# Performance work log

Hardware: AMD Instinct MI355X
Metric: run time of the kernel (lower is better)

The kernel has to match this reference:

```python
import jax, jax.numpy as jnp
import numpy as np

L = 18                      # chain length -> Hilbert dim 2^L
J1 = 1.0                    # fixed exchange coupling (not trainable)
M_KRYLOV = 64               # Lanczos subspace size (>= n_eigs)
DIM = 2 ** L

# spin-1/2 operators (S = sigma/2)
SX = 0.5 * jnp.array([[0., 1.], [1., 0.]], jnp.float32)
SZ = 0.5 * jnp.array([[1., 0.], [0., -1.]], jnp.float32)
# two-site Heisenberg bond S_i.S_j in basis |00>,|01>,|10>,|11> (real: SxSx+SySy = flip terms)
BOND = jnp.array([[0.25, 0., 0., 0.],
                  [0., -0.25, 0.5, 0.],
                  [0., 0.5, -0.25, 0.],
                  [0., 0., 0., 0.25]], jnp.float32)


def setup_inputs() -> dict:
    key = jax.random.key(0)
    phi = jnp.asarray(2.0 * np.pi * np.arange(L) / L, jnp.float32)
    phi = phi + 0.01 * jax.random.normal(key, (L,), jnp.float32)
    return {
        "B_0": jnp.float32(0.2),
        "B_ext": jnp.float32(0.05),
        "phi_i": phi,
        "n_eigs": 4,
    }


def _matvec(v, field_ops):
    """Matrix-free H @ v for the open Heisenberg chain with site fields.
    v: (DIM,), field_ops: (L, 2, 2)."""
    out = jnp.zeros_like(v)
    bond = jnp.float32(J1) * BOND
    for i in range(L - 1):  # fixed structural loop over bonds
        blk = v.reshape(2 ** i, 4, 2 ** (L - i - 2))
        out = out + jnp.einsum('ab,xbz->xaz', bond, blk).reshape(-1)
    for i in range(L):      # fixed structural loop over sites (Zeeman term)
        blk = v.reshape(2 ** i, 2, 2 ** (L - i - 1))
        out = out + jnp.einsum('ab,xbz->xaz', field_ops[i], blk).reshape(-1)
    return out


def _lanczos(field_ops, v0, m):
    """m-step Lanczos; returns Krylov basis V (m, DIM) and tridiag coeffs."""
    def step(carry, _):
        v_prev, v, beta_prev = carry
        w = _matvec(v, field_ops)
        alpha = jnp.vdot(v, w)
        w = w - alpha * v - beta_prev * v_prev
        beta = jnp.sqrt(jnp.vdot(w, w))
        v_next = w / jnp.maximum(beta, jnp.float32(1e-12))
        return (v, v_next, beta), (v, alpha, beta)

    init = (jnp.zeros_like(v0), v0, jnp.float32(0.0))
    _, (V, alphas, betas) = jax.lax.scan(step, init, None, length=m)
    return V, alphas, betas


def reference(B_0, B_ext, phi_i, n_eigs):
    # skyrmion-texture field: in-plane/out-of-plane components from phi_i
    Bx = B_0 * jnp.sin(phi_i)
    Bz = B_0 * jnp.cos(phi_i) + B_ext
    field_ops = Bx[:, None, None] * SX + Bz[:, None, None] * SZ  # (L,2,2)

    v0 = jax.random.normal(jax.random.key(42), (DIM,), jnp.float32)  # v_init='randn'
    v0 = v0 / jnp.sqrt(jnp.vdot(v0, v0))

    V, a, b = _lanczos(field_ops, v0, M_KRYLOV)
    T = jnp.diag(a) + jnp.diag(b[:-1], 1) + jnp.diag(b[:-1], -1)  # (m,m) tridiag
    w, U = jnp.linalg.eigh(T)
    eigvals = w[:n_eigs]                                   # lowest n_eigs Ritz values
    eigvecs = jnp.einsum('md,mk->dk', V, U[:, :n_eigs])    # Ritz vectors (DIM, n_eigs)
    return eigvals, eigvecs
```

## Files before the change

kernel.cpp:

```cpp
#include <hip/hip_runtime.h>
#include <stdint.h>

#define L 18
#define DIM (1 << L)
#define MKRY 64
#define NBLK 256
#define TPB 1024

__device__ __forceinline__ uint32_t rotl32(uint32_t v, int r){ return (v<<r)|(v>>(32-r)); }

__device__ __forceinline__ void threefry2x32(uint32_t k0, uint32_t k1, uint32_t x0, uint32_t x1,
                                             uint32_t& o0, uint32_t& o1) {
  uint32_t k2 = k0 ^ k1 ^ 0x1BD11BDAu;
  x0 += k0; x1 += k1;
  x0+=x1; x1=rotl32(x1,13); x1^=x0;
  x0+=x1; x1=rotl32(x1,15); x1^=x0;
  x0+=x1; x1=rotl32(x1,26); x1^=x0;
  x0+=x1; x1=rotl32(x1,6);  x1^=x0;
  x0+=k1; x1+=k2+1u;
  x0+=x1; x1=rotl32(x1,17); x1^=x0;
  x0+=x1; x1=rotl32(x1,29); x1^=x0;
  x0+=x1; x1=rotl32(x1,16); x1^=x0;
  x0+=x1; x1=rotl32(x1,24); x1^=x0;
  x0+=k2; x1+=k0+2u;
  x0+=x1; x1=rotl32(x1,13); x1^=x0;
  x0+=x1; x1=rotl32(x1,15); x1^=x0;
  x0+=x1; x1=rotl32(x1,26); x1^=x0;
  x0+=x1; x1=rotl32(x1,6);  x1^=x0;
  x0+=k0; x1+=k1+3u;
  x0+=x1; x1=rotl32(x1,17); x1^=x0;
  x0+=x1; x1=rotl32(x1,29); x1^=x0;
  x0+=x1; x1=rotl32(x1,16); x1^=x0;
  x0+=x1; x1=rotl32(x1,24); x1^=x0;
  x0+=k1; x1+=k2+4u;
  x0+=x1; x1=rotl32(x1,13); x1^=x0;
  x0+=x1; x1=rotl32(x1,15); x1^=x0;
  x0+=x1; x1=rotl32(x1,26); x1^=x0;
  x0+=x1; x1=rotl32(x1,6);  x1^=x0;
  x0+=k2; x1+=k0+5u;
  o0=x0; o1=x1;
}

__device__ float jax_erfinv(float x){
  #pragma clang fp contract(off)
  float w = -log1pf(-x*x);
  float p;
  if (w < 5.0f) {
    w = w - 2.5f;
    p = 2.81022636e-08f;
    p = 3.43273939e-07f + p*w;
    p = -3.5233877e-06f + p*w;
    p = -4.39150654e-06f + p*w;
    p = 0.00021858087f + p*w;
    p = -0.00125372503f + p*w;
    p = -0.00417768164f + p*w;
    p = 0.246640727f + p*w;
    p = 1.50140941f + p*w;
  } else {
    w = sqrtf(w) - 3.0f;
    p = -0.000200214257f;
    p = 0.000100950558f + p*w;
    p = 0.00134934322f + p*w;
    p = -0.00367342844f + p*w;
    p = 0.00573950773f + p*w;
    p = -0.0076224613f + p*w;
    p = 0.00943887047f + p*w;
    p = 1.00167406f + p*w;
    p = 2.83297682f + p*w;
  }
  return p*x;
}

__device__ __forceinline__ float rng_val(unsigned i){
  #pragma clang fp contract(off)
  uint32_t o0,o1; threefry2x32(0u,42u,0u,i,o0,o1);
  uint32_t bits = o0 ^ o1;
  float f = __uint_as_float((bits >> 9) | 0x3f800000u) - 1.0f;
  const float lo = -0.99999994f;
  float u = f*2.0f;
  u = u + lo;
  u = fmaxf(lo, u);
  return 1.41421354f * jax_erfinv(u);
}

__device__ __forceinline__ double2 blockReduce2(double a, double b){
  __shared__ double sa[16], sb[16], res[2];
  int lane = threadIdx.x & 63, wid = threadIdx.x >> 6;
  #pragma unroll
  for (int off=32; off; off>>=1){ a += __shfl_down(a,off,64); b += __shfl_down(b,off,64); }
  if (lane==0){ sa[wid]=a; sb[wid]=b; }
  __syncthreads();
  if (wid==0){
    double xa = (lane<16)? sa[lane] : 0.0;
    double xb = (lane<16)? sb[lane] : 0.0;
    #pragma unroll
    for (int off=8; off; off>>=1){ xa += __shfl_down(xa,off,64); xb += __shfl_down(xb,off,64); }
    if (lane==0){ res[0]=xa; res[1]=xb; }
  }
  __syncthreads();
  double2 r; r.x=res[0]; r.y=res[1];
  return r;
}

__device__ __forceinline__ void gbar2(unsigned* bar, unsigned epoch){
  __syncthreads();
  if (threadIdx.x==0){
    const int st = (blockIdx.x & 7)*32;
    __hip_atomic_fetch_add(&bar[st], 1u, __ATOMIC_ACQ_REL, __HIP_MEMORY_SCOPE_AGENT);
    if (blockIdx.x==0){
      unsigned guard=0;
      for (;;){
        unsigned sum=0;
        #pragma unroll
        for (int k=0;k<8;++k)
          sum += __hip_atomic_load(&bar[k*32], __ATOMIC_ACQUIRE, __HIP_MEMORY_SCOPE_AGENT);
        if (sum >= (unsigned)NBLK) break;
        __builtin_amdgcn_s_sleep(1);
        if (++guard > (1u<<22)) break;
      }
      #pragma unroll
      for (int k=0;k<8;++k)
        __hip_atomic_store(&bar[k*32], 0u, __ATOMIC_RELAXED, __HIP_MEMORY_SCOPE_AGENT);
      __hip_atomic_fetch_add(&bar[256], 1u, __ATOMIC_RELEASE, __HIP_MEMORY_SCOPE_AGENT);
    } else {
      unsigned guard=0;
      while (__hip_atomic_load(&bar[256], __ATOMIC_RELAXED, __HIP_MEMORY_SCOPE_AGENT) < epoch){
        __builtin_amdgcn_s_sleep(1);
        if (++guard > (1u<<22)) break;
      }
      (void)__hip_atomic_load(&bar[256], __ATOMIC_ACQUIRE, __HIP_MEMORY_SCOPE_AGENT);
    }
  }
  __syncthreads();
}

__device__ __forceinline__ void gbar_arrive_spin0(unsigned* bar){
  const int st = (blockIdx.x & 7)*32;
  __hip_atomic_fetch_add(&bar[st], 1u, __ATOMIC_ACQ_REL, __HIP_MEMORY_SCOPE_AGENT);
  if (blockIdx.x==0){
    unsigned guard=0;
    for (;;){
      unsigned sum=0;
      #pragma unroll
      for (int k=0;k<8;++k)
        sum += __hip_atomic_load(&bar[k*32], __ATOMIC_ACQUIRE, __HIP_MEMORY_SCOPE_AGENT);
      if (sum >= (unsigned)NBLK) break;
      __builtin_amdgcn_s_sleep(1);
      if (++guard > (1u<<22)) break;
    }
    #pragma unroll
    for (int k=0;k<8;++k)
      __hip_atomic_store(&bar[k*32], 0u, __ATOMIC_RELAXED, __HIP_MEMORY_SCOPE_AGENT);
  }
}

#define CM_INIT {3u<<16,3u<<15,3u<<14,3u<<13,3u<<12,3u<<11,3u<<10,3u<<9, \
                 1u<<17,1u<<16,1u<<15,1u<<14,1u<<13,1u<<12,1u<<11,1u<<10}

__device__ __forceinline__ float matvec1(int s, int tid, float vs,
                                         const float* __restrict__ lds_v,
                                         const float2 (*__restrict__ lds_h)[TPB],
                                         const float* __restrict__ hxz){
  #pragma clang fp contract(off)
  float acc = 0.0f;
  #pragma unroll
  for (int i=0;i<L-1;++i){
    const int q = L-2-i;
    const unsigned msk = 3u<<q;
    const unsigned b2 = ((unsigned)s >> q) & 3u;
    float nbv;
    if (i<=7) nbv = lds_h[i][tid].x;
    else      nbv = lds_v[((unsigned)s ^ msk) & (TPB-1u)];
    if (b2==0u || b2==3u){ acc = acc + 0.25f*vs; }
    else if (b2==1u){ float t = -0.25f*vs; t = t + 0.5f*nbv; acc = acc + t; }
    else            { float t = 0.5f*nbv; t = t + (-0.25f)*vs; acc = acc + t; }
  }
  #pragma unroll
  for (int i=0;i<L;++i){
    const int p = L-1-i;
    const unsigned msk = 1u<<p;
    const float hx = hxz[i], hz = hxz[18+i];
    float nbv;
    if (i<=7) nbv = lds_h[8+i][tid].x;
    else      nbv = lds_v[((unsigned)s ^ msk) & (TPB-1u)];
    float t;
    if ((unsigned)s & msk){ t = hx*nbv; t = t + (-hz)*vs; }
    else                  { t = hz*vs;  t = t + hx*nbv; }
    acc = acc + t;
  }
  return acc;
}


__global__ void k_init(unsigned* bar){ int t=threadIdx.x; if (t<512) bar[t]=0u; }

__global__ void __launch_bounds__(TPB) k_pass1(const float* __restrict__ B0,
        const float* __restrict__ Bext, const float* __restrict__ phi,
        float* __restrict__ vbase, int vmod, float* __restrict__ wring,
        double* __restrict__ part, float* scal, unsigned* bar){
  __shared__ float lds_v[TPB];
  __shared__ float2 lds_h[16][TPB];
  __shared__ float lds_hxz[36];
  const unsigned CM[16] = CM_INIT;
  const int tid = threadIdx.x, bid = blockIdx.x;
  const int s = bid*TPB + tid;

  if (bid==0 && tid < L){
    #pragma clang fp contract(off)
    float b0 = B0[0], be = Bext[0];
    double ph = (double)phi[tid];
    float Bx = b0*(float)sin(ph);
    float Bz = b0*(float)cos(ph);
    Bz = Bz + be;
    scal[130+tid] = 0.5f*Bx;
    scal[148+tid] = 0.5f*Bz;
  }

  float n = rng_val((unsigned)s);
  {
    double2 pr = blockReduce2((double)n*(double)n, 0.0);
    if (tid==0){ part[512+2*bid]=pr.x; part[512+2*bid+1]=pr.y; }
  }
  float nrm;
  if (tid==0) gbar_arrive_spin0(bar);
  if (bid==0){
    __syncthreads();
    double xa = (tid<NBLK)? part[512+2*tid] : 0.0;
    double xb = (tid<NBLK)? part[512+2*tid+1] : 0.0;
    double2 t2 = blockReduce2(xa, xb);
    nrm = (float)sqrt(t2.x);
    if (tid==0){
      scal[129] = nrm;
      __hip_atomic_fetch_add(&bar[256], 1u, __ATOMIC_RELEASE, __HIP_MEMORY_SCOPE_AGENT);
    }
  } else {
    if (tid==0){
      unsigned guard=0;
      while (__hip_atomic_load(&bar[256], __ATOMIC_RELAXED, __HIP_MEMORY_SCOPE_AGENT) < 1u){
        __builtin_amdgcn_s_sleep(1);
        if (++guard > (1u<<22)) break;
      }
      (void)__hip_atomic_load(&bar[256], __ATOMIC_ACQUIRE, __HIP_MEMORY_SCOPE_AGENT);
    }
    __syncthreads();
    nrm = scal[129];
  }

  if (tid < 36) lds_hxz[tid] = scal[130+tid];

  float v = __fdiv_rn(n, nrm), vp = 0.0f, b_p = 0.0f;
  vbase[s] = v;

  #pragma unroll
  for (int ci=0; ci<16; ++ci)
    lds_h[ci][tid] = make_float2(__fdiv_rn(rng_val((unsigned)s ^ CM[ci]), nrm), 0.0f);
  lds_v[tid] = v;
  __syncthreads();

  for (int m=0; m<MKRY; ++m){
    float w = matvec1(s, tid, v, lds_v, lds_h, lds_hxz);
    wring[(size_t)(m&1)*DIM + s] = w;

    double2 p2 = blockReduce2((double)v*(double)w, (double)w*(double)w);
    double* pb = part + (size_t)(m&1)*512;
    if (tid==0){ pb[2*bid]=p2.x; pb[2*bid+1]=p2.y; }

    float alpha, beta;
    if (tid==0) gbar_arrive_spin0(bar);
    if (bid==0){
      __syncthreads();
      double xa = (tid<NBLK)? pb[2*tid] : 0.0;
      double xb = (tid<NBLK)? pb[2*tid+1] : 0.0;
      double2 tt = blockReduce2(xa, xb);
      alpha = (float)tt.x;
      double b2d = tt.y - tt.x*tt.x - (double)b_p*(double)b_p;
      beta = (float)sqrt(fmax(b2d, 0.0));
      if (tid==0){
        scal[m] = alpha; scal[64+m] = beta;
        __hip_atomic_fetch_add(&bar[256], 1u, __ATOMIC_RELEASE, __HIP_MEMORY_SCOPE_AGENT);
      }
    } else {
      if (tid==0){
        unsigned guard=0;
        unsigned ep = 2u + (unsigned)m;
        while (__hip_atomic_load(&bar[256], __ATOMIC_RELAXED, __HIP_MEMORY_SCOPE_AGENT) < ep){
          __builtin_amdgcn_s_sleep(1);
          if (++guard > (1u<<22)) break;
        }
        (void)__hip_atomic_load(&bar[256], __ATOMIC_ACQUIRE, __HIP_MEMORY_SCOPE_AGENT);
      }
      __syncthreads();
      alpha = scal[m]; beta = scal[64+m];
    }
    float bden = fmaxf(beta, 1e-12f);

    float wn[16];
    const float* wr = wring + (size_t)(m&1)*DIM;
    #pragma unroll
    for (int ci=0; ci<16; ++ci) wn[ci] = wr[(unsigned)s ^ CM[ci]];

    float vn;
    {
      #pragma clang fp contract(off)
      float x = w - alpha*v;
      x = x - b_p*vp;
      vn = __fdiv_rn(x, bden);
    }
    vbase[(size_t)((m+1)%vmod)*DIM + s] = vn;

    #pragma unroll
    for (int ci=0; ci<16; ++ci){
      #pragma clang fp contract(off)
      float2 hh = lds_h[ci][tid];
      float x = wn[ci] - alpha*hh.x;
      x = x - b_p*hh.y;
      float hn = __fdiv_rn(x, bden);
      lds_h[ci][tid] = make_float2(hn, hh.x);
    }

    vp=v; v=vn; b_p=beta;
    lds_v[tid]=vn;
    __syncthreads();
  }
}

__global__ void __launch_bounds__(256) k_pass2s(const float* __restrict__ vbase,
        const float* __restrict__ scal, float* __restrict__ out){
  __shared__ float U[256];
  int tid = threadIdx.x;
  int s = blockIdx.x*256 + tid;
  U[tid] = scal[192+tid];
  __syncthreads();
  {
    #pragma clang fp contract(off)
    float o0=0.0f,o1=0.0f,o2=0.0f,o3=0.0f;
    for (int m=0;m<MKRY;++m){
      float vm = vbase[(size_t)m*DIM + s];
      o0 = o0 + vm*U[4*m+0];
      o1 = o1 + vm*U[4*m+1];
      o2 = o2 + vm*U[4*m+2];
      o3 = o3 + vm*U[4*m+3];
    }
    *(float4*)(out + 4 + 4*(size_t)s) = make_float4(o0,o1,o2,o3);
  }
}

__global__ void __launch_bounds__(TPB) k_pass2c(float* __restrict__ wring,
        const float* __restrict__ scal, float* __restrict__ out, unsigned* bar){
  __shared__ float lds_v[TPB];
  __shared__ float2 lds_h[16][TPB];
  __shared__ float lds_hxz[36];
  __shared__ float lds_ab[384];
  const unsigned CM[16] = CM_INIT;
  const int tid = threadIdx.x, bid = blockIdx.x;
  const int s = bid*TPB + tid;
  if (tid < 36) lds_hxz[tid] = scal[130+tid];
  if (tid < 128) lds_ab[tid] = scal[tid];
  if (tid >= 128 && tid < 384) lds_ab[tid] = scal[192 + (tid-128)];
  const float nrm = scal[129];
  float v = __fdiv_rn(rng_val((unsigned)s), nrm), vp = 0.0f;
  #pragma unroll
  for (int ci=0; ci<16; ++ci)
    lds_h[ci][tid] = make_float2(__fdiv_rn(rng_val((unsigned)s ^ CM[ci]), nrm), 0.0f);
  lds_v[tid] = v;
  __syncthreads();
  float o0=0.0f,o1=0.0f,o2=0.0f,o3=0.0f;
  for (int m=0;m<MKRY;++m){
    float w = matvec1(s, tid, v, lds_v, lds_h, lds_hxz);
    wring[(size_t)(m&1)*DIM + s] = w;
    {
      #pragma clang fp contract(off)
      o0 = o0 + v*lds_ab[128+4*m+0];
      o1 = o1 + v*lds_ab[128+4*m+1];
      o2 = o2 + v*lds_ab[128+4*m+2];
      o3 = o3 + v*lds_ab[128+4*m+3];
    }
    gbar2(bar, 66+(unsigned)m);
    float wn[16];
    const float* wr = wring + (size_t)(m&1)*DIM;
    #pragma unroll
    for (int ci=0; ci<16; ++ci) wn[ci] = wr[(unsigned)s ^ CM[ci]];
    float alpha = lds_ab[m];
    float bp = (m==0)? 0.0f : lds_ab[64+m-1];
    float bden = fmaxf(lds_ab[64+m], 1e-12f);
    float vn;
    {
      #pragma clang fp contract(off)
      float x = w - alpha*v;
      x = x - bp*vp;
      vn = __fdiv_rn(x, bden);
    }
    #pragma unroll
    for (int ci=0; ci<16; ++ci){
      #pragma clang fp contract(off)
      float2 hh = lds_h[ci][tid];
      float x = wn[ci] - alpha*hh.x;
      x = x - bp*hh.y;
      float hn = __fdiv_rn(x, bden);
      lds_h[ci][tid] = make_float2(hn, hh.x);
    }
    vp=v; v=vn;
    lds_v[tid]=vn;
    __syncthreads();
  }
  *(float4*)(out + 4 + 4*(size_t)s) = make_float4(o0,o1,o2,o3);
}

__global__ void k_eigh(float* __restrict__ scal, float* __restrict__ out){
  __shared__ double Z[64][65];
  int t = threadIdx.x;
  double ddv = (double)scal[t];
  double eev = (t<63)? (double)scal[64+t] : 0.0;
  for (int j=0;j<64;++j) Z[t][j] = (t==j)?1.0:0.0;
  __syncthreads();

  for (int l=0;l<64;++l){
    for (int iter=0; iter<80; ++iter){
      double dt1 = __shfl_down(ddv, 1, 64);
      bool cond = (t>=l) && (t<63) &&
                  (fabs(eev) <= 2.220446049250313e-16 * (fabs(ddv)+fabs(dt1)));
      unsigned long long bm = __ballot(cond) | (1ull<<63);
      int m = (int)__builtin_ctzll(bm);
      if (m==l) break;
      double dd_l  = __shfl(ddv, l, 64);
      double dd_l1 = __shfl(ddv, l+1, 64);
      double dd_m  = __shfl(ddv, m, 64);
      double ee_l  = __shfl(eev, l, 64);
      double g = (dd_l1-dd_l)/(2.0*ee_l);
      double r = sqrt(fma(g,g,1.0));
      g = dd_m-dd_l + ee_l/(g + copysign(r,g));
      double s=1.0, c=1.0, p=0.0;
      int stop = l;
      double ee_i  = __shfl(eev, m-1, 64);
      double dd_i  = __shfl(ddv, m-1, 64);
      double dd_i1 = dd_m;
      double zhi = Z[t][m];
      for (int i=m-1; i>=l; --i){
        double ee_n=0.0, dd_n=0.0;
        if (i>l){ ee_n = __shfl(eev, i-1, 64); dd_n = __shfl(ddv, i-1, 64); }
        double f = s*ee_i, b = c*ee_i;
        double h = fma(f,f,g*g);
        if (h==0.0){
          if (t==i+1) ddv = dd_i1 - p;
          if (t==m) eev = 0.0;
          stop = i+1;
          break;
        }
        double inv;
        if (h < 1e-35){
          inv = 1.0/sqrt(h);
        } else {
          double x0 = (double)__frsqrt_rn((float)h);
          inv = x0*(1.5 - (0.5*h)*(x0*x0));
        }
        s = f*inv; c = g*inv;
        double rr = h*inv;
        g = dd_i1 - p;
        double r2 = (dd_i - g)*s + 2.0*c*b;
        p = s*r2;
        double ddw = g + p;
        g = c*r2 - b;
        if (t==i+1){ ddv = ddw; eev = rr; }
        double zlo = Z[t][i];
        Z[t][i+1] = s*zlo + c*zhi;
        zhi = c*zlo - s*zhi;
        dd_i1 = dd_i; ee_i = ee_n; dd_i = dd_n;
        if (i==l){
          if (t==l){ ddv = ddv - p; eev = g; }
          if (t==m){ eev = 0.0; }
        }
      }
      Z[t][stop] = zhi;
      __syncthreads();
    }
  }
  double dvm = ddv;
  #pragma unroll
  for (int k=0;k<4;++k){
    double mv = dvm; int mi = t;
    #pragma unroll
    for (int off=32; off; off>>=1){
      double ov = __shfl_down(mv, off, 64);
      int    oi = __shfl_down(mi, off, 64);
      if (ov < mv || (ov==mv && oi<mi)){ mv=ov; mi=oi; }
    }
    int jm = __shfl(mi, 0, 64);
    double lv = __shfl(mv, 0, 64);
    if (t==jm) dvm = 1.0e300;
    scal[192 + t*4 + k] = (float)Z[t][jm];
    if (t==k) out[k] = (float)lv;
  }
}

extern "C" void kernel_launch(void* const* d_in, const int* in_sizes, int n_in,
                              void* d_out, int out_size, void* d_ws, size_t ws_size,
                              hipStream_t stream){
  (void)in_sizes; (void)n_in; (void)out_size;
  const float* B0   = (const float*)d_in[0];
  const float* Bext = (const float*)d_in[1];
  const float* phi  = (const float*)d_in[2];
  float* out = (float*)d_out;

  size_t need_big = ((size_t)(MKRY+3)*DIM)*4 + 16384;
  int vmod; bool big;
  if (ws_size >= need_big) { vmod = MKRY+1; big = true; }
  else                     { vmod = 3;      big = false; }

  float* vbase = (float*)d_ws;
  float* wring = vbase + (size_t)vmod*DIM;
  double* part = (double*)(wring + 2*(size_t)DIM);
  float* scal  = (float*)(part + 1024);
  unsigned* bar = (unsigned*)(scal + 512);

  hipLaunchKernelGGL(k_init, dim3(1), dim3(512), 0, stream, bar);
  {
    void* args[] = { (void*)&B0, (void*)&Bext, (void*)&phi,
                     (void*)&vbase, (void*)&vmod, (void*)&wring,
                     (void*)&part, (void*)&scal, (void*)&bar };
    (void)hipLaunchCooperativeKernel((const void*)k_pass1, dim3(NBLK), dim3(TPB), args, 0, stream);
  }
  hipLaunchKernelGGL(k_eigh, dim3(1), dim3(64), 0, stream, scal, out);
  if (big){
    hipLaunchKernelGGL(k_pass2s, dim3(DIM/256), dim3(256), 0, stream, vbase, scal, out);
  } else {
    void* args[] = { (void*)&wring, (void*)&scal, (void*)&out, (void*)&bar };
    (void)hipLaunchCooperativeKernel((const void*)k_pass2c, dim3(NBLK), dim3(TPB), args, 0, stream);
  }
}
```

Baseline: 2.420 ms.

## Split grid barrier into arrival and reduce-done phases, overlap neighbor loads

The per-iteration grid barrier in the Lanczos pass becomes monotonic arrival counters that are never reset. Block 0 signals a separate 'all arrived' counter, so other blocks can load the 16 neighbour w values from global memory while block 0 is still reducing alpha and beta. The float2 history array in LDS is split into two separate float arrays, and the fallback cooperative kernel gets its own barrier region. This is meant to hide global-load latency behind the serial reduction, at the cost of one extra spin wait per iteration.

Measured after the change: 2.368 ms. -2.2%, faster.

```diff
diff --git a/kernel.cpp b/kernel.cpp
--- a/kernel.cpp
+++ b/kernel.cpp
@@ -102,6 +102,31 @@
   return r;
 }
 
+__device__ __forceinline__ void p1_arrive(unsigned* bar){
+  __hip_atomic_fetch_add(&bar[(blockIdx.x & 7)*32], 1u, __ATOMIC_ACQ_REL, __HIP_MEMORY_SCOPE_AGENT);
+}
+__device__ __forceinline__ void p1_wait_arrivals(unsigned* bar, unsigned target){
+  unsigned guard=0;
+  for (;;){
+    unsigned sum=0;
+    #pragma unroll
+    for (int k=0;k<8;++k)
+      sum += __hip_atomic_load(&bar[k*32], __ATOMIC_RELAXED, __HIP_MEMORY_SCOPE_AGENT);
+    if (sum >= target) break;
+    __builtin_amdgcn_s_sleep(1);
+    if (++guard > (1u<<22)) break;
+  }
+  (void)__hip_atomic_load(&bar[0], __ATOMIC_ACQUIRE, __HIP_MEMORY_SCOPE_AGENT);
+}
+__device__ __forceinline__ void p1_spin(unsigned* ctr, unsigned target){
+  unsigned guard=0;
+  while (__hip_atomic_load(ctr, __ATOMIC_RELAXED, __HIP_MEMORY_SCOPE_AGENT) < target){
+    __builtin_amdgcn_s_sleep(1);
+    if (++guard > (1u<<22)) break;
+  }
+  (void)__hip_atomic_load(ctr, __ATOMIC_ACQUIRE, __HIP_MEMORY_SCOPE_AGENT);
+}
+
 __device__ __forceinline__ void gbar2(unsigned* bar, unsigned epoch){
   __syncthreads();
   if (threadIdx.x==0){
@@ -134,32 +159,12 @@
   __syncthreads();
 }
 
-__device__ __forceinline__ void gbar_arrive_spin0(unsigned* bar){
-  const int st = (blockIdx.x & 7)*32;
-  __hip_atomic_fetch_add(&bar[st], 1u, __ATOMIC_ACQ_REL, __HIP_MEMORY_SCOPE_AGENT);
-  if (blockIdx.x==0){
-    unsigned guard=0;
-    for (;;){
-      unsigned sum=0;
-      #pragma unroll
-      for (int k=0;k<8;++k)
-        sum += __hip_atomic_load(&bar[k*32], __ATOMIC_ACQUIRE, __HIP_MEMORY_SCOPE_AGENT);
-      if (sum >= (unsigned)NBLK) break;
-      __builtin_amdgcn_s_sleep(1);
-      if (++guard > (1u<<22)) break;
-    }
-    #pragma unroll
-    for (int k=0;k<8;++k)
-      __hip_atomic_store(&bar[k*32], 0u, __ATOMIC_RELAXED, __HIP_MEMORY_SCOPE_AGENT);
-  }
-}
-
 #define CM_INIT {3u<<16,3u<<15,3u<<14,3u<<13,3u<<12,3u<<11,3u<<10,3u<<9, \
                  1u<<17,1u<<16,1u<<15,1u<<14,1u<<13,1u<<12,1u<<11,1u<<10}
 
 __device__ __forceinline__ float matvec1(int s, int tid, float vs,
                                          const float* __restrict__ lds_v,
-                                         const float2 (*__restrict__ lds_h)[TPB],
+                                         const float (*__restrict__ lds_hv)[TPB],
                                          const float* __restrict__ hxz){
   #pragma clang fp contract(off)
   float acc = 0.0f;
@@ -169,7 +174,7 @@
     const unsigned msk = 3u<<q;
     const unsigned b2 = ((unsigned)s >> q) & 3u;
     float nbv;
-    if (i<=7) nbv = lds_h[i][tid].x;
+    if (i<=7) nbv = lds_hv[i][tid];
     else      nbv = lds_v[((unsigned)s ^ msk) & (TPB-1u)];
     if (b2==0u || b2==3u){ acc = acc + 0.25f*vs; }
     else if (b2==1u){ float t = -0.25f*vs; t = t + 0.5f*nbv; acc = acc + t; }
@@ -181,7 +186,7 @@
     const unsigned msk = 1u<<p;
     const float hx = hxz[i], hz = hxz[18+i];
     float nbv;
-    if (i<=7) nbv = lds_h[8+i][tid].x;
+    if (i<=7) nbv = lds_hv[8+i][tid];
     else      nbv = lds_v[((unsigned)s ^ msk) & (TPB-1u)];
     float t;
     if ((unsigned)s & msk){ t = hx*nbv; t = t + (-hz)*vs; }
@@ -192,14 +197,15 @@
 }
 
 
-__global__ void k_init(unsigned* bar){ int t=threadIdx.x; if (t<512) bar[t]=0u; }
+__global__ void k_init(unsigned* bar){ int t=threadIdx.x; if (t<1024) bar[t]=0u; }
 
 __global__ void __launch_bounds__(TPB) k_pass1(const float* __restrict__ B0,
         const float* __restrict__ Bext, const float* __restrict__ phi,
         float* __restrict__ vbase, int vmod, float* __restrict__ wring,
         double* __restrict__ part, float* scal, unsigned* bar){
   __shared__ float lds_v[TPB];
-  __shared__ float2 lds_h[16][TPB];
+  __shared__ float lds_hv[16][TPB];
+  __shared__ float lds_hvp[16][TPB];
   __shared__ float lds_hxz[36];
   const unsigned CM[16] = CM_INIT;
   const int tid = threadIdx.x, bid = blockIdx.x;
@@ -222,8 +228,12 @@
     if (tid==0){ part[512+2*bid]=pr.x; part[512+2*bid+1]=pr.y; }
   }
   float nrm;
-  if (tid==0) gbar_arrive_spin0(bar);
   if (bid==0){
+    if (tid==0){
+      p1_arrive(bar);
+      p1_wait_arrivals(bar, (unsigned)NBLK*1u);
+      __hip_atomic_fetch_add(&bar[288], 1u, __ATOMIC_RELEASE, __HIP_MEMORY_SCOPE_AGENT);
+    }
     __syncthreads();
     double xa = (tid<NBLK)? part[512+2*tid] : 0.0;
     double xb = (tid<NBLK)? part[512+2*tid+1] : 0.0;
@@ -235,12 +245,8 @@
     }
   } else {
     if (tid==0){
-      unsigned guard=0;
-      while (__hip_atomic_load(&bar[256], __ATOMIC_RELAXED, __HIP_MEMORY_SCOPE_AGENT) < 1u){
-        __builtin_amdgcn_s_sleep(1);
-        if (++guard > (1u<<22)) break;
-      }
-      (void)__hip_atomic_load(&bar[256], __ATOMIC_ACQUIRE, __HIP_MEMORY_SCOPE_AGENT);
+      p1_arrive(bar);
+      p1_spin(&bar[256], 1u);
     }
     __syncthreads();
     nrm = scal[129];
@@ -252,22 +258,32 @@
   vbase[s] = v;
 
   #pragma unroll
-  for (int ci=0; ci<16; ++ci)
-    lds_h[ci][tid] = make_float2(__fdiv_rn(rng_val((unsigned)s ^ CM[ci]), nrm), 0.0f);
+  for (int ci=0; ci<16; ++ci){
+    lds_hv[ci][tid]  = __fdiv_rn(rng_val((unsigned)s ^ CM[ci]), nrm);
+    lds_hvp[ci][tid] = 0.0f;
+  }
   lds_v[tid] = v;
   __syncthreads();
 
   for (int m=0; m<MKRY; ++m){
-    float w = matvec1(s, tid, v, lds_v, lds_h, lds_hxz);
+    float w = matvec1(s, tid, v, lds_v, lds_hv, lds_hxz);
     wring[(size_t)(m&1)*DIM + s] = w;
 
     double2 p2 = blockReduce2((double)v*(double)w, (double)w*(double)w);
     double* pb = part + (size_t)(m&1)*512;
     if (tid==0){ pb[2*bid]=p2.x; pb[2*bid+1]=p2.y; }
 
+    const unsigned e = 2u + (unsigned)m;
+    const float* wr = wring + (size_t)(m&1)*DIM;
+    float wn[16];
     float alpha, beta;
-    if (tid==0) gbar_arrive_spin0(bar);
+
     if (bid==0){
+      if (tid==0){
+        p1_arrive(bar);
+        p1_wait_arrivals(bar, (unsigned)NBLK*e);
+        __hip_atomic_fetch_add(&bar[288], 1u, __ATOMIC_RELEASE, __HIP_MEMORY_SCOPE_AGENT);
+      }
       __syncthreads();
       double xa = (tid<NBLK)? pb[2*tid] : 0.0;
       double xb = (tid<NBLK)? pb[2*tid+1] : 0.0;
@@ -279,25 +295,23 @@
         scal[m] = alpha; scal[64+m] = beta;
         __hip_atomic_fetch_add(&bar[256], 1u, __ATOMIC_RELEASE, __HIP_MEMORY_SCOPE_AGENT);
       }
+      #pragma unroll
+      for (int ci=0; ci<16; ++ci) wn[ci] = wr[(unsigned)s ^ CM[ci]];
     } else {
       if (tid==0){
-        unsigned guard=0;
-        unsigned ep = 2u + (unsigned)m;
-        while (__hip_atomic_load(&bar[256], __ATOMIC_RELAXED, __HIP_MEMORY_SCOPE_AGENT) < ep){
-          __builtin_amdgcn_s_sleep(1);
-          if (++guard > (1u<<22)) break;
-        }
-        (void)__hip_atomic_load(&bar[256], __ATOMIC_ACQUIRE, __HIP_MEMORY_SCOPE_AGENT);
+        p1_arrive(bar);
+        p1_spin(&bar[288], e);
+      }
+      __syncthreads();
+      #pragma unroll
+      for (int ci=0; ci<16; ++ci) wn[ci] = wr[(unsigned)s ^ CM[ci]];
+      if (tid==0){
+        p1_spin(&bar[256], e);
       }
       __syncthreads();
       alpha = scal[m]; beta = scal[64+m];
     }
     float bden = fmaxf(beta, 1e-12f);
-
-    float wn[16];
-    const float* wr = wring + (size_t)(m&1)*DIM;
-    #pragma unroll
-    for (int ci=0; ci<16; ++ci) wn[ci] = wr[(unsigned)s ^ CM[ci]];
 
     float vn;
     {
@@ -311,11 +325,12 @@
     #pragma unroll
     for (int ci=0; ci<16; ++ci){
       #pragma clang fp contract(off)
-      float2 hh = lds_h[ci][tid];
-      float x = wn[ci] - alpha*hh.x;
-      x = x - b_p*hh.y;
+      float hv = lds_hv[ci][tid];
+      float x = wn[ci] - alpha*hv;
+      x = x - b_p*lds_hvp[ci][tid];
       float hn = __fdiv_rn(x, bden);
-      lds_h[ci][tid] = make_float2(hn, hh.x);
+      lds_hvp[ci][tid] = hv;
+      lds_hv[ci][tid] = hn;
     }
 
     vp=v; v=vn; b_p=beta;
@@ -346,9 +361,10 @@
 }
 
 __global__ void __launch_bounds__(TPB) k_pass2c(float* __restrict__ wring,
-        const float* __restrict__ scal, float* __restrict__ out, unsigned* bar){
+        const float* __restrict__ scal, float* __restrict__ out, unsigned* barc){
   __shared__ float lds_v[TPB];
-  __shared__ float2 lds_h[16][TPB];
+  __shared__ float lds_hv[16][TPB];
+  __shared__ float lds_hvp[16][TPB];
   __shared__ float lds_hxz[36];
   __shared__ float lds_ab[384];
   const unsigned CM[16] = CM_INIT;
@@ -360,13 +376,15 @@
   const float nrm = scal[129];
   float v = __fdiv_rn(rng_val((unsigned)s), nrm), vp = 0.0f;
   #pragma unroll
-  for (int ci=0; ci<16; ++ci)
-    lds_h[ci][tid] = make_float2(__fdiv_rn(rng_val((unsigned)s ^ CM[ci]), nrm), 0.0f);
+  for (int ci=0; ci<16; ++ci){
+    lds_hv[ci][tid]  = __fdiv_rn(rng_val((unsigned)s ^ CM[ci]), nrm);
+    lds_hvp[ci][tid] = 0.0f;
+  }
   lds_v[tid] = v;
   __syncthreads();
   float o0=0.0f,o1=0.0f,o2=0.0f,o3=0.0f;
   for (int m=0;m<MKRY;++m){
-    float w = matvec1(s, tid, v, lds_v, lds_h, lds_hxz);
+    float w = matvec1(s, tid, v, lds_v, lds_hv, lds_hxz);
     wring[(size_t)(m&1)*DIM + s] = w;
     {
       #pragma clang fp contract(off)
@@ -375,7 +393,7 @@
       o2 = o2 + v*lds_ab[128+4*m+2];
       o3 = o3 + v*lds_ab[128+4*m+3];
     }
-    gbar2(bar, 66+(unsigned)m);
+    gbar2(barc, 1+(unsigned)m);
     float wn[16];
     const float* wr = wring + (size_t)(m&1)*DIM;
     #pragma unroll
@@ -393,11 +411,12 @@
     #pragma unroll
     for (int ci=0; ci<16; ++ci){
       #pragma clang fp contract(off)
-      float2 hh = lds_h[ci][tid];
-      float x = wn[ci] - alpha*hh.x;
-      x = x - bp*hh.y;
+      float hv = lds_hv[ci][tid];
+      float x = wn[ci] - alpha*hv;
+      x = x - bp*lds_hvp[ci][tid];
       float hn = __fdiv_rn(x, bden);
-      lds_h[ci][tid] = make_float2(hn, hh.x);
+      lds_hvp[ci][tid] = hv;
+      lds_hv[ci][tid] = hn;
     }
     vp=v; v=vn;
     lds_v[tid]=vn;
@@ -512,7 +531,7 @@
   float* scal  = (float*)(part + 1024);
   unsigned* bar = (unsigned*)(scal + 512);
 
-  hipLaunchKernelGGL(k_init, dim3(1), dim3(512), 0, stream, bar);
+  hipLaunchKernelGGL(k_init, dim3(1), dim3(1024), 0, stream, bar);
   {
     void* args[] = { (void*)&B0, (void*)&Bext, (void*)&phi,
                      (void*)&vbase, (void*)&vmod, (void*)&wring,
@@ -523,7 +542,8 @@
   if (big){
     hipLaunchKernelGGL(k_pass2s, dim3(DIM/256), dim3(256), 0, stream, vbase, scal, out);
   } else {
-    void* args[] = { (void*)&wring, (void*)&scal, (void*)&out, (void*)&bar };
+    unsigned* barc = bar + 512;
+    void* args[] = { (void*)&wring, (void*)&scal, (void*)&out, (void*)&barc };
     (void)hipLaunchCooperativeKernel((const void*)k_pass2c, dim3(NBLK), dim3(TPB), args, 0, stream);
   }
 }
```
